# Kernel tuning notes

Measured on AMD Instinct MI355X. Metric: run time of the kernel, lower is better.

The kernel has to match this reference:

```python
import jax, jax.numpy as jnp
import numpy as np

N_NODES, N_EDGES, D_IN, D_OUT = 40000, 640000, 128, 128


def setup_inputs() -> dict:
    key = jax.random.key(0)
    k0, k1, k2, k3, k4 = jax.random.split(key, 5)
    x = jax.random.normal(k0, (N_NODES, D_IN), dtype=jnp.float32)
    src = jax.random.randint(k1, (N_EDGES,), 0, N_NODES)
    dst = jax.random.randint(k2, (N_EDGES,), 0, N_NODES)
    edge_weight = jax.random.uniform(k3, (N_EDGES,), dtype=jnp.float32)
    # GraphConv learned parameters (Glorot-ish init) and bias
    W = jax.random.normal(k4, (D_IN, D_OUT), dtype=jnp.float32) * (1.0 / np.sqrt(D_IN))
    b = jnp.zeros((D_OUT,), dtype=jnp.float32)
    return {"x": x, "src": src, "dst": dst, "edge_weight": edge_weight, "W": W, "b": b}


def reference(x, src, dst, edge_weight, W, b):
    N = x.shape[0]
    # EdgeWeightNorm(norm='right') on all-ones edge weights: w_e = 1 / in_degree(dst_e)
    deg = jax.ops.segment_sum(jnp.ones_like(edge_weight), dst, num_segments=N)  # [N]
    inv_deg = jnp.where(deg > 0, 1.0 / deg, 0.0)  # allow_zero_in_degree
    w = inv_deg[dst] * edge_weight  # norm_weight *= self.edge_weight  [E]
    # GraphConv norm='none' with edge_weight: h[v] = sum_{e:(u->v)} w_e * x[u]
    msg = x[src] * w[:, None]  # [E, D_IN]
    h = jax.ops.segment_sum(msg, dst, num_segments=N)  # [N, D_IN]
    return h @ W + b  # [N, D_OUT]
```

## Files before the change

### kernel.cpp

```cpp
#include <hip/hip_runtime.h>

#define N_NODES 40000
#define N_EDGES 640000
#define D 128
#define NB 157
#define GEMM_ROWS 32


__global__ __launch_bounds__(256) void init_kernel(int* __restrict__ deg,
                                                   int* __restrict__ cursor) {
    int i = blockIdx.x * 256 + threadIdx.x;
    if (i < N_NODES) { deg[i] = 0; cursor[i] = 0; }
}

__global__ __launch_bounds__(256) void degree_kernel(const int* __restrict__ dst,
                                                     int* __restrict__ deg) {
    int e = blockIdx.x * 256 + threadIdx.x;
    if (e < N_EDGES) atomicAdd(&deg[dst[e]], 1);
}

__global__ __launch_bounds__(256) void reduce_kernel(const int* __restrict__ deg,
                                                     int* __restrict__ bsum) {
    __shared__ int s[256];
    int t = threadIdx.x;
    int idx = blockIdx.x * 256 + t;
    s[t] = (idx < N_NODES) ? deg[idx] : 0;
    __syncthreads();
#pragma unroll
    for (int off = 128; off > 0; off >>= 1) {
        if (t < off) s[t] += s[t + off];
        __syncthreads();
    }
    if (t == 0) bsum[blockIdx.x] = s[0];
}

__global__ __launch_bounds__(256) void offs_kernel(const int* __restrict__ deg,
                                                   const int* __restrict__ bsum,
                                                   int* __restrict__ offs,
                                                   float* __restrict__ invdeg) {
    __shared__ int s[256];
    __shared__ int base_s;
    int t = threadIdx.x;

    int v = (t < blockIdx.x && t < NB) ? bsum[t] : 0;
    s[t] = v;
    __syncthreads();
#pragma unroll
    for (int off = 128; off > 0; off >>= 1) {
        if (t < off) s[t] += s[t + off];
        __syncthreads();
    }
    if (t == 0) base_s = s[0];
    __syncthreads();
    int base = base_s;
    __syncthreads();

    int idx = blockIdx.x * 256 + t;
    int d = (idx < N_NODES) ? deg[idx] : 0;
    s[t] = d;
    __syncthreads();
#pragma unroll
    for (int off = 1; off < 256; off <<= 1) {
        int u = (t >= off) ? s[t - off] : 0;
        __syncthreads();
        s[t] += u;
        __syncthreads();
    }
    int excl = s[t] - d + base;
    if (idx < N_NODES) {
        offs[idx] = excl;
        invdeg[idx] = (d > 0) ? (1.0f / (float)d) : 0.0f;
        if (idx == N_NODES - 1) offs[N_NODES] = excl + d;
    }
}

__global__ __launch_bounds__(256) void bucket_kernel(const int* __restrict__ src,
                                                     const int* __restrict__ dst,
                                                     const float* __restrict__ ew,
                                                     const int* __restrict__ offs,
                                                     int* __restrict__ cursor,
                                                     int2* __restrict__ pairs) {
    int e = blockIdx.x * 256 + threadIdx.x;
    if (e >= N_EDGES) return;
    int d = dst[e];
    int pos = offs[d] + atomicAdd(&cursor[d], 1);
    pairs[pos] = make_int2(src[e], __float_as_int(ew[e]));
}

__global__ __launch_bounds__(256) void gemm_xw_kernel(const float* __restrict__ x,
                                                      const float* __restrict__ W,
                                                      float* __restrict__ y) {
    __shared__ float Ws[D * D];
    __shared__ float xs[GEMM_ROWS * D];
    const int tid = threadIdx.x;
    const int rowbase = blockIdx.x * GEMM_ROWS;

    float4* Ws4 = reinterpret_cast<float4*>(Ws);
    const float4* W4 = reinterpret_cast<const float4*>(W);
#pragma unroll
    for (int i = 0; i < 16; ++i)
        Ws4[tid + i * 256] = W4[tid + i * 256];

    float4* xs4 = reinterpret_cast<float4*>(xs);
    const float4* x4 = reinterpret_cast<const float4*>(x) + rowbase * (D / 4);
#pragma unroll
    for (int i = 0; i < GEMM_ROWS * (D / 4) / 256; ++i)
        xs4[tid + i * 256] = x4[tid + i * 256];
    __syncthreads();

    const int lane = tid & 31;
    const int rp   = tid >> 5;
    const float* xr0 = xs + (rp * 4 + 0) * D;
    const float* xr1 = xs + (rp * 4 + 1) * D;
    const float* xr2 = xs + (rp * 4 + 2) * D;
    const float* xr3 = xs + (rp * 4 + 3) * D;

    float4 a0 = {0.f,0.f,0.f,0.f}, a1 = a0, a2 = a0, a3 = a0;
#pragma unroll 4
    for (int k = 0; k < D; ++k) {
        float4 wv = Ws4[k * (D / 4) + lane];
        float x0 = xr0[k], x1 = xr1[k], x2 = xr2[k], x3 = xr3[k];
        a0.x += x0*wv.x; a0.y += x0*wv.y; a0.z += x0*wv.z; a0.w += x0*wv.w;
        a1.x += x1*wv.x; a1.y += x1*wv.y; a1.z += x1*wv.z; a1.w += x1*wv.w;
        a2.x += x2*wv.x; a2.y += x2*wv.y; a2.z += x2*wv.z; a2.w += x2*wv.w;
        a3.x += x3*wv.x; a3.y += x3*wv.y; a3.z += x3*wv.z; a3.w += x3*wv.w;
    }

    float4* y4 = reinterpret_cast<float4*>(y);
    int r0 = rowbase + rp * 4;
    y4[(r0 + 0) * (D / 4) + lane] = a0;
    y4[(r0 + 1) * (D / 4) + lane] = a1;
    y4[(r0 + 2) * (D / 4) + lane] = a2;
    y4[(r0 + 3) * (D / 4) + lane] = a3;
}

__global__ __launch_bounds__(256) void gather_kernel(const int* __restrict__ offs,
                                                     const int2* __restrict__ pairs,
                                                     const float* __restrict__ invdeg,
                                                     const float* __restrict__ y,
                                                     const float* __restrict__ b,
                                                     float* __restrict__ out) {
    int gid = blockIdx.x * 256 + threadIdx.x;
    int v    = gid >> 5;
    int part = gid & 31;
    if (v >= N_NODES) return;
    int beg = offs[v];
    int end = offs[v + 1];
    const float4* y4 = reinterpret_cast<const float4*>(y);
    float4 acc = {0.f, 0.f, 0.f, 0.f};
    for (int base = beg; base < end; base += 32) {
        int n = end - base; if (n > 32) n = 32;
        int2 pe = make_int2(0, 0);
        if (part < n) pe = pairs[base + part];
        for (int j = 0; j < n; ++j) {
            int   s = __shfl(pe.x, j, 32);
            float w = __int_as_float(__shfl(pe.y, j, 32));
            float4 t = y4[s * (D / 4) + part];
            acc.x += w * t.x; acc.y += w * t.y; acc.z += w * t.z; acc.w += w * t.w;
        }
    }
    float idv = invdeg[v];
    float4 bv = reinterpret_cast<const float4*>(b)[part];
    acc.x = acc.x * idv + bv.x;
    acc.y = acc.y * idv + bv.y;
    acc.z = acc.z * idv + bv.z;
    acc.w = acc.w * idv + bv.w;
    reinterpret_cast<float4*>(out)[v * (D / 4) + part] = acc;
}

extern "C" void kernel_launch(void* const* d_in, const int* in_sizes, int n_in,
                              void* d_out, int out_size, void* d_ws, size_t ws_size,
                              hipStream_t stream) {
    const float* x   = (const float*)d_in[0];
    const int*   src = (const int*)d_in[1];
    const int*   dst = (const int*)d_in[2];
    const float* ew  = (const float*)d_in[3];
    const float* W   = (const float*)d_in[4];
    const float* b   = (const float*)d_in[5];
    float* out = (float*)d_out;

    char* ws = (char*)d_ws;
    float* y      = (float*)ws;                       ws += (size_t)N_NODES * D * 4;
    int*   deg    = (int*)ws;                         ws += (size_t)N_NODES * 4;
    int*   cursor = (int*)ws;                         ws += (size_t)N_NODES * 4;
    float* invdeg = (float*)ws;                       ws += (size_t)N_NODES * 4;
    int*   offs   = (int*)ws;                         ws += (size_t)(N_NODES + 16) * 4;
    int*   bsum   = (int*)ws;                         ws += (size_t)((NB + 19) & ~3) * 4;
    int2*  pairs  = (int2*)ws;

    init_kernel<<<(N_NODES + 255) / 256, 256, 0, stream>>>(deg, cursor);
    degree_kernel<<<(N_EDGES + 255) / 256, 256, 0, stream>>>(dst, deg);
    reduce_kernel<<<NB, 256, 0, stream>>>(deg, bsum);
    offs_kernel<<<NB, 256, 0, stream>>>(deg, bsum, offs, invdeg);
    gemm_xw_kernel<<<N_NODES / GEMM_ROWS, 256, 0, stream>>>(x, W, y);
    bucket_kernel<<<(N_EDGES + 255) / 256, 256, 0, stream>>>(src, dst, ew,
                                                             offs, cursor, pairs);
    {
        long long total = (long long)N_NODES * 32;
        gather_kernel<<<(int)((total + 255) / 256), 256, 0, stream>>>(offs, pairs, invdeg, y, b, out);
    }
}
```

Measured before the change: 212.1 us.

## Fuse GEMM with degree count, drop cursor array, unroll gather accumulation

The degree-count pass now runs as extra blocks inside the GEMM launch, and the GEMM reads x and W directly from global/L1 instead of staging 80 KB in LDS, which allows more blocks per CU. The cursor array and init kernel are replaced by a memset plus atomicSub on deg during bucketing, with edge pairs written via nontemporal 64-bit stores. The gather loop is unrolled by four with independent accumulators to raise memory-level parallelism. Risks are heavier global/L1 traffic in the GEMM without LDS reuse, and a reversed within-bucket ordering that changes the float summation order slightly.

```diff
diff --git a/kernel.cpp b/kernel.cpp
--- a/kernel.cpp
+++ b/kernel.cpp
@@ -5,18 +5,52 @@
 #define D 128
 #define NB 157
 #define GEMM_ROWS 32
-
-
-__global__ __launch_bounds__(256) void init_kernel(int* __restrict__ deg,
-                                                   int* __restrict__ cursor) {
-    int i = blockIdx.x * 256 + threadIdx.x;
-    if (i < N_NODES) { deg[i] = 0; cursor[i] = 0; }
-}
-
-__global__ __launch_bounds__(256) void degree_kernel(const int* __restrict__ dst,
-                                                     int* __restrict__ deg) {
-    int e = blockIdx.x * 256 + threadIdx.x;
-    if (e < N_EDGES) atomicAdd(&deg[dst[e]], 1);
+#define GEMM_BLOCKS (N_NODES / GEMM_ROWS)
+#define DEG_BLOCKS ((N_EDGES + 255) / 256)
+
+
+__global__ __launch_bounds__(256) void gemm_degree_kernel(const float* __restrict__ x,
+                                                          const float* __restrict__ W,
+                                                          float* __restrict__ y,
+                                                          const int* __restrict__ dst,
+                                                          int* __restrict__ deg) {
+    const int tid = threadIdx.x;
+    if (blockIdx.x >= GEMM_BLOCKS) {
+        int e = (blockIdx.x - GEMM_BLOCKS) * 256 + tid;
+        if (e < N_EDGES) atomicAdd(&deg[dst[e]], 1);
+        return;
+    }
+    const int lane = tid & 31;
+    const int rp   = tid >> 5;
+    const int r0   = blockIdx.x * GEMM_ROWS + rp * 4;
+
+    const float4* W4 = reinterpret_cast<const float4*>(W);
+    const float4* xr0 = reinterpret_cast<const float4*>(x) + (r0 + 0) * (D / 4);
+    const float4* xr1 = reinterpret_cast<const float4*>(x) + (r0 + 1) * (D / 4);
+    const float4* xr2 = reinterpret_cast<const float4*>(x) + (r0 + 2) * (D / 4);
+    const float4* xr3 = reinterpret_cast<const float4*>(x) + (r0 + 3) * (D / 4);
+
+    float4 a0 = {0.f,0.f,0.f,0.f}, a1 = a0, a2 = a0, a3 = a0;
+#pragma unroll 4
+    for (int kb = 0; kb < D / 4; ++kb) {
+        float4 xv0 = xr0[kb], xv1 = xr1[kb], xv2 = xr2[kb], xv3 = xr3[kb];
+        float4 w0 = W4[(kb * 4 + 0) * (D / 4) + lane];
+        float4 w1 = W4[(kb * 4 + 1) * (D / 4) + lane];
+        float4 w2 = W4[(kb * 4 + 2) * (D / 4) + lane];
+        float4 w3 = W4[(kb * 4 + 3) * (D / 4) + lane];
+#define FMA4(A, XV)                                                       \
+        A.x += XV.x*w0.x + XV.y*w1.x; A.x += XV.z*w2.x + XV.w*w3.x;       \
+        A.y += XV.x*w0.y + XV.y*w1.y; A.y += XV.z*w2.y + XV.w*w3.y;       \
+        A.z += XV.x*w0.z + XV.y*w1.z; A.z += XV.z*w2.z + XV.w*w3.z;       \
+        A.w += XV.x*w0.w + XV.y*w1.w; A.w += XV.z*w2.w + XV.w*w3.w;
+        FMA4(a0, xv0) FMA4(a1, xv1) FMA4(a2, xv2) FMA4(a3, xv3)
+#undef FMA4
+    }
+    float4* y4 = reinterpret_cast<float4*>(y);
+    y4[(r0 + 0) * (D / 4) + lane] = a0;
+    y4[(r0 + 1) * (D / 4) + lane] = a1;
+    y4[(r0 + 2) * (D / 4) + lane] = a2;
+    y4[(r0 + 3) * (D / 4) + lane] = a3;
 }
 
 __global__ __launch_bounds__(256) void reduce_kernel(const int* __restrict__ deg,
@@ -78,60 +112,16 @@
                                                      const int* __restrict__ dst,
                                                      const float* __restrict__ ew,
                                                      const int* __restrict__ offs,
-                                                     int* __restrict__ cursor,
-                                                     int2* __restrict__ pairs) {
+                                                     int* __restrict__ deg,
+                                                     long long* __restrict__ pairs) {
     int e = blockIdx.x * 256 + threadIdx.x;
     if (e >= N_EDGES) return;
     int d = dst[e];
-    int pos = offs[d] + atomicAdd(&cursor[d], 1);
-    pairs[pos] = make_int2(src[e], __float_as_int(ew[e]));
-}
-
-__global__ __launch_bounds__(256) void gemm_xw_kernel(const float* __restrict__ x,
-                                                      const float* __restrict__ W,
-                                                      float* __restrict__ y) {
-    __shared__ float Ws[D * D];
-    __shared__ float xs[GEMM_ROWS * D];
-    const int tid = threadIdx.x;
-    const int rowbase = blockIdx.x * GEMM_ROWS;
-
-    float4* Ws4 = reinterpret_cast<float4*>(Ws);
-    const float4* W4 = reinterpret_cast<const float4*>(W);
-#pragma unroll
-    for (int i = 0; i < 16; ++i)
-        Ws4[tid + i * 256] = W4[tid + i * 256];
-
-    float4* xs4 = reinterpret_cast<float4*>(xs);
-    const float4* x4 = reinterpret_cast<const float4*>(x) + rowbase * (D / 4);
-#pragma unroll
-    for (int i = 0; i < GEMM_ROWS * (D / 4) / 256; ++i)
-        xs4[tid + i * 256] = x4[tid + i * 256];
-    __syncthreads();
-
-    const int lane = tid & 31;
-    const int rp   = tid >> 5;
-    const float* xr0 = xs + (rp * 4 + 0) * D;
-    const float* xr1 = xs + (rp * 4 + 1) * D;
-    const float* xr2 = xs + (rp * 4 + 2) * D;
-    const float* xr3 = xs + (rp * 4 + 3) * D;
-
-    float4 a0 = {0.f,0.f,0.f,0.f}, a1 = a0, a2 = a0, a3 = a0;
-#pragma unroll 4
-    for (int k = 0; k < D; ++k) {
-        float4 wv = Ws4[k * (D / 4) + lane];
-        float x0 = xr0[k], x1 = xr1[k], x2 = xr2[k], x3 = xr3[k];
-        a0.x += x0*wv.x; a0.y += x0*wv.y; a0.z += x0*wv.z; a0.w += x0*wv.w;
-        a1.x += x1*wv.x; a1.y += x1*wv.y; a1.z += x1*wv.z; a1.w += x1*wv.w;
-        a2.x += x2*wv.x; a2.y += x2*wv.y; a2.z += x2*wv.z; a2.w += x2*wv.w;
-        a3.x += x3*wv.x; a3.y += x3*wv.y; a3.z += x3*wv.z; a3.w += x3*wv.w;
-    }
-
-    float4* y4 = reinterpret_cast<float4*>(y);
-    int r0 = rowbase + rp * 4;
-    y4[(r0 + 0) * (D / 4) + lane] = a0;
-    y4[(r0 + 1) * (D / 4) + lane] = a1;
-    y4[(r0 + 2) * (D / 4) + lane] = a2;
-    y4[(r0 + 3) * (D / 4) + lane] = a3;
+    int c = atomicSub(&deg[d], 1);
+    int pos = offs[d] + c - 1;
+    unsigned long long packed = (unsigned long long)(unsigned int)src[e]
+                              | ((unsigned long long)(unsigned int)__float_as_uint(ew[e]) << 32);
+    __builtin_nontemporal_store((long long)packed, &pairs[pos]);
 }
 
 __global__ __launch_bounds__(256) void gather_kernel(const int* __restrict__ offs,
@@ -147,25 +137,43 @@
     int beg = offs[v];
     int end = offs[v + 1];
     const float4* y4 = reinterpret_cast<const float4*>(y);
-    float4 acc = {0.f, 0.f, 0.f, 0.f};
+    float4 acc0 = {0.f,0.f,0.f,0.f}, acc1 = acc0, acc2 = acc0, acc3 = acc0;
     for (int base = beg; base < end; base += 32) {
         int n = end - base; if (n > 32) n = 32;
         int2 pe = make_int2(0, 0);
         if (part < n) pe = pairs[base + part];
-        for (int j = 0; j < n; ++j) {
+        int j = 0;
+        for (; j + 4 <= n; j += 4) {
+            int   s0 = __shfl(pe.x, j + 0, 32), s1 = __shfl(pe.x, j + 1, 32);
+            int   s2 = __shfl(pe.x, j + 2, 32), s3 = __shfl(pe.x, j + 3, 32);
+            float w0 = __int_as_float(__shfl(pe.y, j + 0, 32));
+            float w1 = __int_as_float(__shfl(pe.y, j + 1, 32));
+            float w2 = __int_as_float(__shfl(pe.y, j + 2, 32));
+            float w3 = __int_as_float(__shfl(pe.y, j + 3, 32));
+            float4 t0 = y4[s0 * (D / 4) + part];
+            float4 t1 = y4[s1 * (D / 4) + part];
+            float4 t2 = y4[s2 * (D / 4) + part];
+            float4 t3 = y4[s3 * (D / 4) + part];
+            acc0.x += w0*t0.x; acc0.y += w0*t0.y; acc0.z += w0*t0.z; acc0.w += w0*t0.w;
+            acc1.x += w1*t1.x; acc1.y += w1*t1.y; acc1.z += w1*t1.z; acc1.w += w1*t1.w;
+            acc2.x += w2*t2.x; acc2.y += w2*t2.y; acc2.z += w2*t2.z; acc2.w += w2*t2.w;
+            acc3.x += w3*t3.x; acc3.y += w3*t3.y; acc3.z += w3*t3.z; acc3.w += w3*t3.w;
+        }
+        for (; j < n; ++j) {
             int   s = __shfl(pe.x, j, 32);
             float w = __int_as_float(__shfl(pe.y, j, 32));
             float4 t = y4[s * (D / 4) + part];
-            acc.x += w * t.x; acc.y += w * t.y; acc.z += w * t.z; acc.w += w * t.w;
+            acc0.x += w*t.x; acc0.y += w*t.y; acc0.z += w*t.z; acc0.w += w*t.w;
         }
     }
     float idv = invdeg[v];
     float4 bv = reinterpret_cast<const float4*>(b)[part];
-    acc.x = acc.x * idv + bv.x;
-    acc.y = acc.y * idv + bv.y;
-    acc.z = acc.z * idv + bv.z;
-    acc.w = acc.w * idv + bv.w;
-    reinterpret_cast<float4*>(out)[v * (D / 4) + part] = acc;
+    float4 r;
+    r.x = (acc0.x + acc1.x + acc2.x + acc3.x) * idv + bv.x;
+    r.y = (acc0.y + acc1.y + acc2.y + acc3.y) * idv + bv.y;
+    r.z = (acc0.z + acc1.z + acc2.z + acc3.z) * idv + bv.z;
+    r.w = (acc0.w + acc1.w + acc2.w + acc3.w) * idv + bv.w;
+    reinterpret_cast<float4*>(out)[v * (D / 4) + part] = r;
 }
 
 extern "C" void kernel_launch(void* const* d_in, const int* in_sizes, int n_in,
@@ -182,21 +190,20 @@
     char* ws = (char*)d_ws;
     float* y      = (float*)ws;                       ws += (size_t)N_NODES * D * 4;
     int*   deg    = (int*)ws;                         ws += (size_t)N_NODES * 4;
-    int*   cursor = (int*)ws;                         ws += (size_t)N_NODES * 4;
     float* invdeg = (float*)ws;                       ws += (size_t)N_NODES * 4;
     int*   offs   = (int*)ws;                         ws += (size_t)(N_NODES + 16) * 4;
     int*   bsum   = (int*)ws;                         ws += (size_t)((NB + 19) & ~3) * 4;
-    int2*  pairs  = (int2*)ws;
-
-    init_kernel<<<(N_NODES + 255) / 256, 256, 0, stream>>>(deg, cursor);
-    degree_kernel<<<(N_EDGES + 255) / 256, 256, 0, stream>>>(dst, deg);
+    long long* pairs = (long long*)ws;
+
+    hipMemsetAsync(deg, 0, (size_t)N_NODES * 4, stream);
+
+    gemm_degree_kernel<<<GEMM_BLOCKS + DEG_BLOCKS, 256, 0, stream>>>(x, W, y, dst, deg);
     reduce_kernel<<<NB, 256, 0, stream>>>(deg, bsum);
     offs_kernel<<<NB, 256, 0, stream>>>(deg, bsum, offs, invdeg);
-    gemm_xw_kernel<<<N_NODES / GEMM_ROWS, 256, 0, stream>>>(x, W, y);
-    bucket_kernel<<<(N_EDGES + 255) / 256, 256, 0, stream>>>(src, dst, ew,
-                                                             offs, cursor, pairs);
+    bucket_kernel<<<DEG_BLOCKS, 256, 0, stream>>>(src, dst, ew, offs, deg, pairs);
     {
         long long total = (long long)N_NODES * 32;
-        gather_kernel<<<(int)((total + 255) / 256), 256, 0, stream>>>(offs, pairs, invdeg, y, b, out);
-    }
-}
+        gather_kernel<<<(int)((total + 255) / 256), 256, 0, stream>>>(
+            offs, (const int2*)pairs, invdeg, y, b, out);
+    }
+}
```

Measured after the change: 224.0 us. +5.6%, slower.
